# Performance work log

Measured on AMD Instinct MI355X. Metric: run time of the kernel, lower is better.

Reference implementation:

```python
import jax, jax.numpy as jnp
import numpy as np

N, E, B = 50000, 800000, 512
IN, H, D, C = 128, 4, 64, 1
NG, GH = 200, 256


def gat_layer(h, W, al, ar, src, dst, res_w=None, res_id=False, act=True):
    """DGL-style GATConv: fc -> per-head attn logits -> edge softmax by dst -> scatter-sum."""
    Nn = h.shape[0]
    Hh, Dd = al.shape
    f = (h @ W).reshape(Nn, Hh, Dd)                       # [N,H,D]
    el = jnp.einsum('nhd,hd->nh', f, al)                  # [N,H]
    er = jnp.einsum('nhd,hd->nh', f, ar)
    e = jax.nn.leaky_relu(el[src] + er[dst], 0.2)         # [E,H]
    m = jax.ops.segment_max(e, dst, num_segments=Nn)      # softmax over in-edges of each dst
    ex = jnp.exp(e - m[dst])
    den = jax.ops.segment_sum(ex, dst, num_segments=Nn)
    a = ex / den[dst]                                      # [E,H]
    rst = jax.ops.segment_sum(f[src] * a[..., None], dst, num_segments=Nn)  # [N,H,D]
    if res_id:
        rst = rst + h.reshape(Nn, Hh, Dd)
    elif res_w is not None:
        rst = rst + (h @ res_w).reshape(Nn, Hh, Dd)
    if act:
        rst = jax.nn.elu(rst)
    return rst


def setup_inputs() -> dict:
    key = jax.random.key(0)
    ks = jax.random.split(key, 24)
    s = 0.05
    HD = H * D
    return {
        'feat': jax.random.normal(ks[0], (N, IN), jnp.float32),
        'src': jax.random.randint(ks[1], (E,), 0, N, jnp.int32),
        'dst': jax.random.randint(ks[2], (E,), 0, N, jnp.int32),
        'graph_ids': jnp.sort(jax.random.randint(ks[3], (N,), 0, B, jnp.int32)),
        'g_feat': jax.random.normal(ks[4], (B, NG), jnp.float32),
        'W0': jax.random.normal(ks[5], (IN, HD), jnp.float32) * s,
        'al0': jax.random.normal(ks[6], (H, D), jnp.float32) * s,
        'ar0': jax.random.normal(ks[7], (H, D), jnp.float32) * s,
        'W1': jax.random.normal(ks[8], (HD, HD), jnp.float32) * s,
        'al1': jax.random.normal(ks[9], (H, D), jnp.float32) * s,
        'ar1': jax.random.normal(ks[10], (H, D), jnp.float32) * s,
        'W2': jax.random.normal(ks[11], (HD, HD), jnp.float32) * s,
        'al2': jax.random.normal(ks[12], (H, D), jnp.float32) * s,
        'ar2': jax.random.normal(ks[13], (H, D), jnp.float32) * s,
        'W3': jax.random.normal(ks[14], (HD, H * C), jnp.float32) * s,
        'al3': jax.random.normal(ks[15], (H, C), jnp.float32) * s,
        'ar3': jax.random.normal(ks[16], (H, C), jnp.float32) * s,
        'resW3': jax.random.normal(ks[17], (HD, H * C), jnp.float32) * s,
        'gw1': jax.random.normal(ks[18], (NG, GH), jnp.float32) * s,
        'gb1': jnp.zeros((GH,), jnp.float32),
        'gw2': jax.random.normal(ks[19], (GH, GH), jnp.float32) * s,
        'gb2': jnp.zeros((GH,), jnp.float32),
        'lw': jax.random.normal(ks[20], (H + GH, C), jnp.float32) * s,
        'lb': jnp.zeros((C,), jnp.float32),
    }


def reference(feat, src, dst, graph_ids, g_feat,
              W0, al0, ar0, W1, al1, ar1, W2, al2, ar2,
              W3, al3, ar3, resW3, gw1, gb1, gw2, gb2, lw, lb):
    h = gat_layer(feat, W0, al0, ar0, src, dst).reshape(N, -1)
    h = gat_layer(h, W1, al1, ar1, src, dst, res_id=True).reshape(N, -1)
    h = gat_layer(h, W2, al2, ar2, src, dst, res_id=True).reshape(N, -1)
    hn = gat_layer(h, W3, al3, ar3, src, dst, res_w=resW3, act=False)   # [N,H,C]
    latent = jax.ops.segment_sum(hn, graph_ids, num_segments=B).mean(axis=-1)  # [B,H]
    lg = jax.nn.relu(jax.nn.relu(g_feat @ gw1 + gb1) @ gw2 + gb2)        # [B,GH]
    return jnp.concatenate([latent, lg], axis=1) @ lw + lb               # [B,C]
```

## Files before the change

### kernel.cpp

```cpp
#include <hip/hip_runtime.h>
#include <hip/hip_bf16.h>
#include <math.h>

#define N_NODES 50000
#define N_EDGES 800000
#define NB      512
#define IN_F    128
#define NH      4
#define HD      64
#define HDIM    256
#define NG_F    200
#define GH_F    256
#define CSZ     196

typedef __attribute__((ext_vector_type(8))) short short8;
typedef __attribute__((ext_vector_type(8))) unsigned short u16x8;
typedef __attribute__((ext_vector_type(4))) float f32x4;
typedef __attribute__((ext_vector_type(2))) float f32x2;

static __device__ __forceinline__ float lrelu(float x){ return x > 0.f ? x : 0.2f*x; }
static __device__ __forceinline__ float fexp(float x){ return __expf(x); }

static __device__ __forceinline__ unsigned short f2b(float f){
  union { float f; unsigned int u; } v; v.f = f;
  unsigned int r = v.u + 0x7fffu + ((v.u >> 16) & 1u);
  return (unsigned short)(r >> 16);
}
static __device__ __forceinline__ float b2f(unsigned short b){
  union { unsigned int u; float f; } v; v.u = ((unsigned int)b) << 16;
  return v.f;
}
static __device__ __forceinline__ float u2f(unsigned int u){
  union { unsigned int u; float f; } v; v.u = u;
  return v.f;
}

__global__ __launch_bounds__(256) void k_f2b(const float* __restrict__ in, unsigned short* __restrict__ out, int n4){
  int i = blockIdx.x*256 + threadIdx.x;
  if (i >= n4) return;
  float4 v = ((const float4*)in)[i];
  ushort4 o;
  o.x = f2b(v.x); o.y = f2b(v.y); o.z = f2b(v.z); o.w = f2b(v.w);
  ((ushort4*)out)[i] = o;
}

__global__ __launch_bounds__(256) void k_padg(const float* __restrict__ g, unsigned short* __restrict__ out){
  int idx = blockIdx.x*256 + threadIdx.x;
  if (idx >= NB*256) return;
  int b = idx >> 8, k = idx & 255;
  out[idx] = (k < NG_F) ? f2b(g[b*NG_F + k]) : (unsigned short)0;
}

__global__ __launch_bounds__(256) void k_w2bt(const float* __restrict__ W, unsigned short* __restrict__ Bt,
                                              int Ksrc, int Kdst, int NC){
  __shared__ unsigned short t[32][33];
  int bn = blockIdx.x*32;
  int bk = blockIdx.y*32;
  int lx = threadIdx.x & 31, ly = threadIdx.x >> 5;
  #pragma unroll
  for (int i = 0; i < 32; i += 8) {
    int kr = bk + ly + i;
    t[ly+i][lx] = (kr < Ksrc) ? f2b(W[(size_t)kr*NC + bn+lx]) : (unsigned short)0;
  }
  __syncthreads();
  #pragma unroll
  for (int i = 0; i < 32; i += 8)
    Bt[(size_t)(bn+ly+i)*Kdst + bk+lx] = t[lx][ly+i];
}

__global__ __launch_bounds__(256) void k_hist(const int* __restrict__ dst, int* __restrict__ deg){
  int e = blockIdx.x*256 + threadIdx.x;
  if (e < N_EDGES) atomicAdd(&deg[dst[e]], 1);
}

__global__ __launch_bounds__(64) void k_s1a(const int* __restrict__ deg, int* __restrict__ blocksum){
  int b = blockIdx.x, lane = threadIdx.x;
  int start = b*CSZ, end = min(start+CSZ, N_NODES);
  int s = 0;
  for (int i = start + lane; i < end; i += 64) s += deg[i];
  #pragma unroll
  for (int m = 1; m < 64; m <<= 1) s += __shfl_xor(s, m);
  if (lane == 0) blocksum[b] = s;
}

__global__ __launch_bounds__(256) void k_s1b(const int* __restrict__ blocksum, int* __restrict__ chunkoff){
  __shared__ int sd[256];
  int t = threadIdx.x;
  int own = blocksum[t];
  sd[t] = own; __syncthreads();
  for (int off = 1; off < 256; off <<= 1) {
    int v = (t >= off) ? sd[t-off] : 0;
    __syncthreads();
    sd[t] += v;
    __syncthreads();
  }
  chunkoff[t] = sd[t] - own;
}

__global__ __launch_bounds__(64) void k_scan2(const int* __restrict__ deg, const int* __restrict__ chunkoff,
                                              int* __restrict__ row_start, int* __restrict__ cursor){
  int b = blockIdx.x, lane = threadIdx.x;
  int start = b*CSZ, end = min(start+CSZ, N_NODES);
  int run = chunkoff[b];
  for (int k = start; k < end; k += 64) {
    int idx = k + lane;
    int v = (idx < end) ? deg[idx] : 0;
    int inc = v;
    #pragma unroll
    for (int off = 1; off < 64; off <<= 1) {
      int t = __shfl_up(inc, off);
      if (lane >= off) inc += t;
    }
    int excl = run + inc - v;
    if (idx < end) { row_start[idx] = excl; cursor[idx] = excl; }
    run += __shfl(inc, 63);
  }
  if (b == 255 && lane == 0) row_start[N_NODES] = run;
}

__global__ __launch_bounds__(256) void k_scatter(const int* __restrict__ dst, const int* __restrict__ src,
                                                 int* __restrict__ cursor, int* __restrict__ csrc){
  int e = blockIdx.x*256 + threadIdx.x;
  if (e < N_EDGES) {
    int p = atomicAdd(&cursor[dst[e]], 1);
    csrc[p] = src[e];
  }
}

__global__ __launch_bounds__(256) void k_goff(const int* __restrict__ gid, int* __restrict__ goff){
  int n = blockIdx.x*256 + threadIdx.x;
  if (n >= N_NODES) return;
  int ca = gid[n];
  if (n == 0) {
    for (int g = 0; g <= ca; g++) goff[g] = 0;
  } else {
    int pa = gid[n-1];
    for (int g = pa+1; g <= ca; g++) goff[g] = n;
  }
  if (n == N_NODES-1) {
    for (int g = ca+1; g <= NB; g++) goff[g] = N_NODES;
  }
}

__global__ __launch_bounds__(256) void k_gemm_bf16(const unsigned short* __restrict__ A,
                                                   const unsigned short* __restrict__ Bt,
                                                   unsigned short* __restrict__ C,
                                                   const float* __restrict__ bias, int act,
                                                   int M, int K, int NC){
  __shared__ unsigned short As[128][72];
  __shared__ unsigned short Bs[64][72];
  const int tid = threadIdx.x;
  const int bm = blockIdx.y*128, bn = blockIdx.x*64;
  const int wid = tid >> 6, lane = tid & 63;
  const int wr = wid >> 1, wc = wid & 1;
  const int l15 = lane & 15, lg = lane >> 4;
  const int ar = tid >> 1, ak = (tid & 1) * 32;
  const int br = tid >> 2, bkp = (tid & 3) * 16;
  int agrow = bm + ar; if (agrow >= M) agrow = M - 1;

  f32x4 acc[4][2] = {};
  for (int k0 = 0; k0 < K; k0 += 64) {
    #pragma unroll
    for (int p = 0; p < 4; p++)
      *(uint4*)(&As[ar][ak + p*8]) = *(const uint4*)(A + (size_t)agrow*K + k0 + ak + p*8);
    #pragma unroll
    for (int p = 0; p < 2; p++)
      *(uint4*)(&Bs[br][bkp + p*8]) = *(const uint4*)(Bt + (size_t)(bn + br)*K + k0 + bkp + p*8);
    __syncthreads();
    #pragma unroll
    for (int ks = 0; ks < 2; ks++) {
      short8 af[4], bf[2];
      #pragma unroll
      for (int m = 0; m < 4; m++) af[m] = *(const short8*)(&As[wr*64 + m*16 + l15][ks*32 + lg*8]);
      #pragma unroll
      for (int nn = 0; nn < 2; nn++) bf[nn] = *(const short8*)(&Bs[wc*32 + nn*16 + l15][ks*32 + lg*8]);
      #pragma unroll
      for (int m = 0; m < 4; m++)
        #pragma unroll
        for (int nn = 0; nn < 2; nn++)
          acc[m][nn] = __builtin_amdgcn_mfma_f32_16x16x32_bf16(af[m], bf[nn], acc[m][nn], 0, 0, 0);
    }
    __syncthreads();
  }
  #pragma unroll
  for (int m = 0; m < 4; m++)
    #pragma unroll
    for (int nn = 0; nn < 2; nn++) {
      int col = bn + wc*32 + nn*16 + l15;
      float bv = bias ? bias[col] : 0.f;
      #pragma unroll
      for (int i = 0; i < 4; i++) {
        int row = bm + wr*64 + m*16 + lg*4 + i;
        if (row < M) {
          float v = acc[m][nn][i] + bv;
          if (act) v = fmaxf(v, 0.f);
          C[(size_t)row*NC + col] = f2b(v);
        }
      }
    }
}

__global__ __launch_bounds__(256) void k_logits(const unsigned short* __restrict__ f,
    const float* __restrict__ al, const float* __restrict__ ar,
    float* __restrict__ el, float* __restrict__ er){
  int n = blockIdx.x*4 + (threadIdx.x >> 6);
  int lane = threadIdx.x & 63;
  if (n >= N_NODES) return;
  ushort4 u = ((const ushort4*)(f + (size_t)n*HDIM))[lane];
  float4 av = ((const float4*)al)[lane];
  float4 rv = ((const float4*)ar)[lane];
  float x0 = b2f(u.x), x1 = b2f(u.y), x2 = b2f(u.z), x3 = b2f(u.w);
  float pl = x0*av.x + x1*av.y + x2*av.z + x3*av.w;
  float pr = x0*rv.x + x1*rv.y + x2*rv.z + x3*rv.w;
  #pragma unroll
  for (int m = 1; m < 16; m <<= 1) {
    pl += __shfl_xor(pl, m);
    pr += __shfl_xor(pr, m);
  }
  if ((lane & 15) == 0) {
    int h = lane >> 4;
    el[n*NH + h] = pl;
    er[n*NH + h] = pr;
  }
}

__global__ __launch_bounds__(256) void k_agg(
    const unsigned short* __restrict__ f, const float* __restrict__ el, const float* __restrict__ er,
    const int* __restrict__ row_start, const int* __restrict__ csrc,
    const unsigned short* __restrict__ resid, unsigned short* __restrict__ out, int act){
  __shared__ float sA[4][64][4];
  __shared__ int   sS[4][64];
  int wid  = threadIdx.x >> 6;
  int lane = threadIdx.x & 63;
  int n = blockIdx.x*4 + wid;
  int half = lane >> 5;
  int c    = lane & 31;
  int h    = c >> 3;
  int e0 = row_start[n], e1 = row_start[n+1];
  float4 erv = ((const float4*)er)[n];

  float4 den = make_float4(0.f,0.f,0.f,0.f);
  f32x2 acc2[4] = {};

  for (int base = e0; base < e1; base += 64) {
    int cnt = min(64, e1 - base);
    int   s_l = 0;
    float4 a4 = make_float4(0.f,0.f,0.f,0.f);
    if (base + lane < e1) {
      s_l = csrc[base + lane];
      float4 ev = ((const float4*)el)[s_l];
      a4.x = fexp(lrelu(ev.x + erv.x));
      a4.y = fexp(lrelu(ev.y + erv.y));
      a4.z = fexp(lrelu(ev.z + erv.z));
      a4.w = fexp(lrelu(ev.w + erv.w));
    }
    den.x += a4.x; den.y += a4.y; den.z += a4.z; den.w += a4.w;
    sS[wid][lane] = s_l;
    sA[wid][lane][0] = a4.x; sA[wid][lane][1] = a4.y;
    sA[wid][lane][2] = a4.z; sA[wid][lane][3] = a4.w;
    __builtin_amdgcn_sched_barrier(0);
    for (int j = 0; j < cnt; j += 16) {
      uint4 u[8]; f32x2 aa[8];
      #pragma unroll
      for (int p = 0; p < 8; p++) {
        int jj = j + 2*p + half;
        float a = 0.f; int s;
        if (jj < cnt) { s = sS[wid][jj]; a = sA[wid][jj][h]; } else { s = sS[wid][j]; }
        u[p] = *(const uint4*)(f + (size_t)s*HDIM + c*8);
        aa[p][0] = a; aa[p][1] = a;
      }
      #pragma unroll
      for (int p = 0; p < 8; p++) {
        f32x2 p0, p1, p2, p3;
        p0[0] = u2f(u[p].x << 16); p0[1] = u2f(u[p].x & 0xffff0000u);
        p1[0] = u2f(u[p].y << 16); p1[1] = u2f(u[p].y & 0xffff0000u);
        p2[0] = u2f(u[p].z << 16); p2[1] = u2f(u[p].z & 0xffff0000u);
        p3[0] = u2f(u[p].w << 16); p3[1] = u2f(u[p].w & 0xffff0000u);
        asm volatile("v_pk_fma_f32 %0, %1, %2, %0" : "+v"(acc2[0]) : "v"(p0), "v"(aa[p]));
        asm volatile("v_pk_fma_f32 %0, %1, %2, %0" : "+v"(acc2[1]) : "v"(p1), "v"(aa[p]));
        asm volatile("v_pk_fma_f32 %0, %1, %2, %0" : "+v"(acc2[2]) : "v"(p2), "v"(aa[p]));
        asm volatile("v_pk_fma_f32 %0, %1, %2, %0" : "+v"(acc2[3]) : "v"(p3), "v"(aa[p]));
      }
    }
  }
  #pragma unroll
  for (int m = 1; m < 64; m <<= 1) {
    den.x += __shfl_xor(den.x, m);
    den.y += __shfl_xor(den.y, m);
    den.z += __shfl_xor(den.z, m);
    den.w += __shfl_xor(den.w, m);
  }
  float accv[8];
  #pragma unroll
  for (int q = 0; q < 4; q++) {
    accv[2*q]   = acc2[q][0] + __shfl_xor(acc2[q][0], 32);
    accv[2*q+1] = acc2[q][1] + __shfl_xor(acc2[q][1], 32);
  }

  float d_h = h==0 ? den.x : h==1 ? den.y : h==2 ? den.z : den.w;
  float inv = d_h > 0.f ? 1.0f/d_h : 0.f;

  if (half == 0) {
    #pragma unroll
    for (int k = 0; k < 8; k++) accv[k] *= inv;
    if (resid) {
      u16x8 r = *(const u16x8*)(resid + (size_t)n*HDIM + c*8);
      #pragma unroll
      for (int k = 0; k < 8; k++) accv[k] += b2f((unsigned short)r[k]);
    }
    if (act) {
      #pragma unroll
      for (int k = 0; k < 8; k++) accv[k] = accv[k] > 0.f ? accv[k] : (fexp(accv[k]) - 1.0f);
    }
    u16x8 o;
    #pragma unroll
    for (int k = 0; k < 8; k++) o[k] = f2b(accv[k]);
    *(u16x8*)(out + (size_t)n*HDIM + c*8) = o;
  }
}

__global__ __launch_bounds__(256) void k_l3proj(const unsigned short* __restrict__ h,
    const float* __restrict__ W3, const float* __restrict__ rW3,
    const float* __restrict__ al3, const float* __restrict__ ar3,
    float* __restrict__ f3, float* __restrict__ r3,
    float* __restrict__ el3, float* __restrict__ er3){
  int n = blockIdx.x*4 + (threadIdx.x >> 6);
  int lane = threadIdx.x & 63;
  if (n >= N_NODES) return;
  ushort4 u = ((const ushort4*)(h + (size_t)n*HDIM))[lane];
  float hk[4] = {b2f(u.x), b2f(u.y), b2f(u.z), b2f(u.w)};
  const float4* w  = (const float4*)W3;
  const float4* rw = (const float4*)rW3;
  float4 acc = make_float4(0.f,0.f,0.f,0.f);
  float4 rac = make_float4(0.f,0.f,0.f,0.f);
  #pragma unroll
  for (int j = 0; j < 4; j++) {
    float4 wv = w[lane*4 + j];
    float4 rv = rw[lane*4 + j];
    acc.x += hk[j]*wv.x; acc.y += hk[j]*wv.y; acc.z += hk[j]*wv.z; acc.w += hk[j]*wv.w;
    rac.x += hk[j]*rv.x; rac.y += hk[j]*rv.y; rac.z += hk[j]*rv.z; rac.w += hk[j]*rv.w;
  }
  #pragma unroll
  for (int m = 1; m < 64; m <<= 1) {
    acc.x += __shfl_xor(acc.x, m); acc.y += __shfl_xor(acc.y, m);
    acc.z += __shfl_xor(acc.z, m); acc.w += __shfl_xor(acc.w, m);
    rac.x += __shfl_xor(rac.x, m); rac.y += __shfl_xor(rac.y, m);
    rac.z += __shfl_xor(rac.z, m); rac.w += __shfl_xor(rac.w, m);
  }
  if (lane == 0) {
    ((float4*)f3)[n] = acc;
    ((float4*)r3)[n] = rac;
    float4 e1 = make_float4(acc.x*al3[0], acc.y*al3[1], acc.z*al3[2], acc.w*al3[3]);
    float4 e2 = make_float4(acc.x*ar3[0], acc.y*ar3[1], acc.z*ar3[2], acc.w*ar3[3]);
    ((float4*)el3)[n] = e1;
    ((float4*)er3)[n] = e2;
  }
}

__global__ __launch_bounds__(256) void k_l3node(
    const float* __restrict__ f3, const float* __restrict__ el3, const float* __restrict__ er3,
    const int* __restrict__ row_start, const int* __restrict__ csrc,
    const float* __restrict__ r3, float* __restrict__ hn){
  int g = threadIdx.x >> 4;
  int l = threadIdx.x & 15;
  int n = blockIdx.x*16 + g;
  int e0 = row_start[n], e1 = row_start[n+1];
  float4 erv = ((const float4*)er3)[n];

  float4 dn  = make_float4(0.f,0.f,0.f,0.f);
  float4 acc = make_float4(0.f,0.f,0.f,0.f);
  for (int i = e0 + l; i < e1; i += 16) {
    int s = csrc[i];
    float4 ev = ((const float4*)el3)[s];
    float ax = fexp(lrelu(ev.x + erv.x));
    float ay = fexp(lrelu(ev.y + erv.y));
    float az = fexp(lrelu(ev.z + erv.z));
    float aw = fexp(lrelu(ev.w + erv.w));
    dn.x += ax; dn.y += ay; dn.z += az; dn.w += aw;
    float4 fv = ((const float4*)f3)[s];
    acc.x += ax*fv.x; acc.y += ay*fv.y; acc.z += az*fv.z; acc.w += aw*fv.w;
  }
  #pragma unroll
  for (int m = 1; m < 16; m <<= 1) {
    dn.x += __shfl_xor(dn.x, m);  dn.y += __shfl_xor(dn.y, m);
    dn.z += __shfl_xor(dn.z, m);  dn.w += __shfl_xor(dn.w, m);
    acc.x += __shfl_xor(acc.x, m); acc.y += __shfl_xor(acc.y, m);
    acc.z += __shfl_xor(acc.z, m); acc.w += __shfl_xor(acc.w, m);
  }
  if (l == 0) {
    float4 rv = ((const float4*)r3)[n];
    float4 o;
    o.x = (dn.x > 0.f ? acc.x/dn.x : 0.f) + rv.x;
    o.y = (dn.y > 0.f ? acc.y/dn.y : 0.f) + rv.y;
    o.z = (dn.z > 0.f ? acc.z/dn.z : 0.f) + rv.z;
    o.w = (dn.w > 0.f ? acc.w/dn.w : 0.f) + rv.w;
    ((float4*)hn)[n] = o;
  }
}

__global__ __launch_bounds__(64) void k_gseg(const float* __restrict__ hn, const int* __restrict__ goff,
                                             float* __restrict__ latent){
  int b = blockIdx.x;
  int lane = threadIdx.x;
  int n0 = goff[b], n1 = goff[b+1];
  float4 s = make_float4(0.f,0.f,0.f,0.f);
  for (int n = n0 + lane; n < n1; n += 64) {
    float4 v = ((const float4*)hn)[n];
    s.x += v.x; s.y += v.y; s.z += v.z; s.w += v.w;
  }
  #pragma unroll
  for (int m = 1; m < 64; m <<= 1) {
    s.x += __shfl_xor(s.x, m); s.y += __shfl_xor(s.y, m);
    s.z += __shfl_xor(s.z, m); s.w += __shfl_xor(s.w, m);
  }
  if (lane == 0) ((float4*)latent)[b] = s;
}

__global__ __launch_bounds__(256) void k_final(const float* __restrict__ latent, const unsigned short* __restrict__ lgb,
    const float* __restrict__ lw, const float* __restrict__ lb, float* __restrict__ out){
  int b = blockIdx.x*4 + (threadIdx.x >> 6);
  int lane = threadIdx.x & 63;
  if (b >= NB) return;
  ushort4 u = ((const ushort4*)(lgb + (size_t)b*GH_F))[lane];
  float4 wv = ((const float4*)(lw + NH))[lane];
  float s = b2f(u.x)*wv.x + b2f(u.y)*wv.y + b2f(u.z)*wv.z + b2f(u.w)*wv.w;
  #pragma unroll
  for (int m = 1; m < 64; m <<= 1) s += __shfl_xor(s, m);
  if (lane == 0) {
    float4 lv = ((const float4*)latent)[b];
    out[b] = s + lv.x*lw[0] + lv.y*lw[1] + lv.z*lw[2] + lv.w*lw[3] + lb[0];
  }
}

__global__ __launch_bounds__(256) void k_sentinel(float* out){
  int i = blockIdx.x*256 + threadIdx.x;
  if (i < NB) out[i] = -12345.0f;
}

extern "C" void kernel_launch(void* const* d_in, const int* in_sizes, int n_in,
                              void* d_out, int out_size, void* d_ws, size_t ws_size,
                              hipStream_t stream){
  const float* feat   = (const float*)d_in[0];
  const int*   src    = (const int*)d_in[1];
  const int*   dst    = (const int*)d_in[2];
  const int*   gid    = (const int*)d_in[3];
  const float* g_feat = (const float*)d_in[4];
  const float* W0   = (const float*)d_in[5];
  const float* al0  = (const float*)d_in[6];
  const float* ar0  = (const float*)d_in[7];
  const float* W1   = (const float*)d_in[8];
  const float* al1  = (const float*)d_in[9];
  const float* ar1  = (const float*)d_in[10];
  const float* W2   = (const float*)d_in[11];
  const float* al2  = (const float*)d_in[12];
  const float* ar2  = (const float*)d_in[13];
  const float* W3   = (const float*)d_in[14];
  const float* al3  = (const float*)d_in[15];
  const float* ar3  = (const float*)d_in[16];
  const float* rW3  = (const float*)d_in[17];
  const float* gw1  = (const float*)d_in[18];
  const float* gb1  = (const float*)d_in[19];
  const float* gw2  = (const float*)d_in[20];
  const float* gb2  = (const float*)d_in[21];
  const float* lw   = (const float*)d_in[22];
  const float* lb   = (const float*)d_in[23];
  float* out = (float*)d_out;

  char* base = (char*)d_ws;
  size_t off = 0;
  auto alloc = [&](size_t bytes)->char* {
    char* r = base + off;
    off += (bytes + 255) & ~(size_t)255;
    return r;
  };
  unsigned short* featb = (unsigned short*)alloc((size_t)N_NODES*IN_F*2);
  unsigned short* fbuf  = (unsigned short*)alloc((size_t)N_NODES*HDIM*2);
  unsigned short* hA    = (unsigned short*)alloc((size_t)N_NODES*HDIM*2);
  unsigned short* hB    = (unsigned short*)alloc((size_t)N_NODES*HDIM*2);
  unsigned short* W0t   = (unsigned short*)alloc((size_t)IN_F*HDIM*2);
  unsigned short* W1t   = (unsigned short*)alloc((size_t)HDIM*HDIM*2);
  unsigned short* W2t   = (unsigned short*)alloc((size_t)HDIM*HDIM*2);
  unsigned short* gfb   = (unsigned short*)alloc((size_t)NB*256*2);
  unsigned short* gw1t  = (unsigned short*)alloc((size_t)GH_F*256*2);
  unsigned short* gw2t  = (unsigned short*)alloc((size_t)GH_F*GH_F*2);
  unsigned short* g1b   = (unsigned short*)alloc((size_t)NB*GH_F*2);
  unsigned short* lgb   = (unsigned short*)alloc((size_t)NB*GH_F*2);
  float* el   = (float*)alloc((size_t)N_NODES*NH*4);
  float* er   = (float*)alloc((size_t)N_NODES*NH*4);
  float* f3   = (float*)alloc((size_t)N_NODES*NH*4);
  float* r3   = (float*)alloc((size_t)N_NODES*NH*4);
  float* hn   = (float*)alloc((size_t)N_NODES*NH*4);
  int* deg       = (int*)alloc((size_t)N_NODES*4);
  int* row_start = (int*)alloc((size_t)(N_NODES+1)*4);
  int* cursor    = (int*)alloc((size_t)N_NODES*4);
  int* csrc      = (int*)alloc((size_t)N_EDGES*4);
  int* blocksum  = (int*)alloc(256*4);
  int* chunkoff  = (int*)alloc(256*4);
  int* goff      = (int*)alloc((size_t)(NB+1)*4);
  float* latent  = (float*)alloc((size_t)NB*NH*4);

  if (off > ws_size) {
    k_sentinel<<<2, 256, 0, stream>>>(out);
    return;
  }

  k_f2b<<<((N_NODES*IN_F/4)+255)/256, 256, 0, stream>>>(feat, featb, N_NODES*IN_F/4);
  {
    dim3 g0(HDIM/32, IN_F/32), g12(HDIM/32, HDIM/32), gm(256/32, 256/32);
    k_w2bt<<<g0, 256, 0, stream>>>(W0, W0t, IN_F, IN_F, HDIM);
    k_w2bt<<<g12, 256, 0, stream>>>(W1, W1t, HDIM, HDIM, HDIM);
    k_w2bt<<<g12, 256, 0, stream>>>(W2, W2t, HDIM, HDIM, HDIM);
    k_w2bt<<<gm, 256, 0, stream>>>(gw1, gw1t, NG_F, 256, GH_F);
    k_w2bt<<<gm, 256, 0, stream>>>(gw2, gw2t, GH_F, GH_F, GH_F);
  }
  k_padg<<<(NB*256+255)/256, 256, 0, stream>>>(g_feat, gfb);

  hipMemsetAsync(deg, 0, (size_t)N_NODES*4, stream);
  k_hist<<<(N_EDGES+255)/256, 256, 0, stream>>>(dst, deg);
  k_s1a<<<256, 64, 0, stream>>>(deg, blocksum);
  k_s1b<<<1, 256, 0, stream>>>(blocksum, chunkoff);
  k_scan2<<<256, 64, 0, stream>>>(deg, chunkoff, row_start, cursor);
  k_scatter<<<(N_EDGES+255)/256, 256, 0, stream>>>(dst, src, cursor, csrc);
  k_goff<<<(N_NODES+255)/256, 256, 0, stream>>>(gid, goff);

  dim3 ggrid(HDIM/64, (N_NODES+127)/128);

  k_gemm_bf16<<<ggrid, 256, 0, stream>>>(featb, W0t, fbuf, nullptr, 0, N_NODES, IN_F, HDIM);
  k_logits<<<(N_NODES+3)/4, 256, 0, stream>>>(fbuf, al0, ar0, el, er);
  k_agg<<<N_NODES/4, 256, 0, stream>>>(fbuf, el, er, row_start, csrc, nullptr, hA, 1);

  k_gemm_bf16<<<ggrid, 256, 0, stream>>>(hA, W1t, fbuf, nullptr, 0, N_NODES, HDIM, HDIM);
  k_logits<<<(N_NODES+3)/4, 256, 0, stream>>>(fbuf, al1, ar1, el, er);
  k_agg<<<N_NODES/4, 256, 0, stream>>>(fbuf, el, er, row_start, csrc, hA, hB, 1);

  k_gemm_bf16<<<ggrid, 256, 0, stream>>>(hB, W2t, fbuf, nullptr, 0, N_NODES, HDIM, HDIM);
  k_logits<<<(N_NODES+3)/4, 256, 0, stream>>>(fbuf, al2, ar2, el, er);
  k_agg<<<N_NODES/4, 256, 0, stream>>>(fbuf, el, er, row_start, csrc, hB, hA, 1);

  k_l3proj<<<(N_NODES+3)/4, 256, 0, stream>>>(hA, W3, rW3, al3, ar3, f3, r3, el, er);
  k_l3node<<<N_NODES/16, 256, 0, stream>>>(f3, el, er, row_start, csrc, r3, hn);
  k_gseg<<<NB, 64, 0, stream>>>(hn, goff, latent);

  {
    dim3 mgrid(GH_F/64, (NB+127)/128);
    k_gemm_bf16<<<mgrid, 256, 0, stream>>>(gfb, gw1t, g1b, gb1, 1, NB, 256, GH_F);
    k_gemm_bf16<<<mgrid, 256, 0, stream>>>(g1b, gw2t, lgb, gb2, 1, NB, GH_F, GH_F);
  }
  k_final<<<(NB+3)/4, 256, 0, stream>>>(latent, lgb, lw, lb, out);
}
```

Baseline: 483.6 us.

## Fuse attention logits into GEMM epilogue and shrink agg gather unroll

The per-head el/er dot products are computed from the fp32 MFMA accumulators inside the GEMM epilogue. Each block owns one head's 64 columns, so partial sums are reduced across lanes and waves through shared memory. This removes the separate k_logits kernel and its re-read of the projected features in three layers. Separately, the k_agg inner gather loop is cut from 8 to 4 outstanding neighbor loads per iteration, trading memory-level parallelism for lower register pressure. The fused epilogue adds shuffles and a block barrier to every GEMM call that supplies attention vectors, and computes the logits from unrounded fp32 values rather than the bf16-rounded stored features.

After: 482.1 us. Within noise of the previous version (-0.3%).

```diff
diff --git a/kernel.cpp b/kernel.cpp
--- a/kernel.cpp
+++ b/kernel.cpp
@@ -146,23 +146,27 @@
                                                    const unsigned short* __restrict__ Bt,
                                                    unsigned short* __restrict__ C,
                                                    const float* __restrict__ bias, int act,
+                                                   const float* __restrict__ al, const float* __restrict__ ar,
+                                                   float* __restrict__ el, float* __restrict__ er,
                                                    int M, int K, int NC){
   __shared__ unsigned short As[128][72];
   __shared__ unsigned short Bs[64][72];
+  __shared__ float sEL[2][2][4][16];
+  __shared__ float sER[2][2][4][16];
   const int tid = threadIdx.x;
   const int bm = blockIdx.y*128, bn = blockIdx.x*64;
   const int wid = tid >> 6, lane = tid & 63;
   const int wr = wid >> 1, wc = wid & 1;
   const int l15 = lane & 15, lg = lane >> 4;
-  const int ar = tid >> 1, ak = (tid & 1) * 32;
+  const int ar_ = tid >> 1, ak = (tid & 1) * 32;
   const int br = tid >> 2, bkp = (tid & 3) * 16;
-  int agrow = bm + ar; if (agrow >= M) agrow = M - 1;
+  int agrow = bm + ar_; if (agrow >= M) agrow = M - 1;
 
   f32x4 acc[4][2] = {};
   for (int k0 = 0; k0 < K; k0 += 64) {
     #pragma unroll
     for (int p = 0; p < 4; p++)
-      *(uint4*)(&As[ar][ak + p*8]) = *(const uint4*)(A + (size_t)agrow*K + k0 + ak + p*8);
+      *(uint4*)(&As[ar_][ak + p*8]) = *(const uint4*)(A + (size_t)agrow*K + k0 + ak + p*8);
     #pragma unroll
     for (int p = 0; p < 2; p++)
       *(uint4*)(&Bs[br][bkp + p*8]) = *(const uint4*)(Bt + (size_t)(bn + br)*K + k0 + bkp + p*8);
@@ -198,29 +202,45 @@
         }
       }
     }
-}
-
-__global__ __launch_bounds__(256) void k_logits(const unsigned short* __restrict__ f,
-    const float* __restrict__ al, const float* __restrict__ ar,
-    float* __restrict__ el, float* __restrict__ er){
-  int n = blockIdx.x*4 + (threadIdx.x >> 6);
-  int lane = threadIdx.x & 63;
-  if (n >= N_NODES) return;
-  ushort4 u = ((const ushort4*)(f + (size_t)n*HDIM))[lane];
-  float4 av = ((const float4*)al)[lane];
-  float4 rv = ((const float4*)ar)[lane];
-  float x0 = b2f(u.x), x1 = b2f(u.y), x2 = b2f(u.z), x3 = b2f(u.w);
-  float pl = x0*av.x + x1*av.y + x2*av.z + x3*av.w;
-  float pr = x0*rv.x + x1*rv.y + x2*rv.z + x3*rv.w;
-  #pragma unroll
-  for (int m = 1; m < 16; m <<= 1) {
-    pl += __shfl_xor(pl, m);
-    pr += __shfl_xor(pr, m);
-  }
-  if ((lane & 15) == 0) {
-    int h = lane >> 4;
-    el[n*NH + h] = pl;
-    er[n*NH + h] = pr;
+  if (al) {
+    int hidx = bn >> 6;
+    float pl[16], pr[16];
+    #pragma unroll
+    for (int m = 0; m < 4; m++)
+      #pragma unroll
+      for (int i = 0; i < 4; i++) {
+        float sl = 0.f, sr = 0.f;
+        #pragma unroll
+        for (int nn = 0; nn < 2; nn++) {
+          int colh = wc*32 + nn*16 + l15;
+          sl += acc[m][nn][i] * al[hidx*64 + colh];
+          sr += acc[m][nn][i] * ar[hidx*64 + colh];
+        }
+        pl[m*4+i] = sl; pr[m*4+i] = sr;
+      }
+    #pragma unroll
+    for (int k = 0; k < 16; k++) {
+      #pragma unroll
+      for (int mm = 1; mm < 16; mm <<= 1) {
+        pl[k] += __shfl_xor(pl[k], mm);
+        pr[k] += __shfl_xor(pr[k], mm);
+      }
+    }
+    if (l15 == 0) {
+      #pragma unroll
+      for (int k = 0; k < 16; k++) { sEL[wr][wc][lg][k] = pl[k]; sER[wr][wc][lg][k] = pr[k]; }
+    }
+    __syncthreads();
+    if (tid < 128) {
+      int k = tid & 15;
+      int lg2 = (tid >> 4) & 3;
+      int wr2 = tid >> 6;
+      float vl = sEL[wr2][0][lg2][k] + sEL[wr2][1][lg2][k];
+      float vr = sER[wr2][0][lg2][k] + sER[wr2][1][lg2][k];
+      int m = k >> 2, i = k & 3;
+      int row = bm + wr2*64 + m*16 + lg2*4 + i;
+      if (row < M) { el[row*NH + hidx] = vl; er[row*NH + hidx] = vr; }
+    }
   }
 }
 
@@ -259,10 +279,10 @@
     sA[wid][lane][0] = a4.x; sA[wid][lane][1] = a4.y;
     sA[wid][lane][2] = a4.z; sA[wid][lane][3] = a4.w;
     __builtin_amdgcn_sched_barrier(0);
-    for (int j = 0; j < cnt; j += 16) {
-      uint4 u[8]; f32x2 aa[8];
-      #pragma unroll
-      for (int p = 0; p < 8; p++) {
+    for (int j = 0; j < cnt; j += 8) {
+      uint4 u[4]; f32x2 aa[4];
+      #pragma unroll
+      for (int p = 0; p < 4; p++) {
         int jj = j + 2*p + half;
         float a = 0.f; int s;
         if (jj < cnt) { s = sS[wid][jj]; a = sA[wid][jj][h]; } else { s = sS[wid][j]; }
@@ -270,7 +290,7 @@
         aa[p][0] = a; aa[p][1] = a;
       }
       #pragma unroll
-      for (int p = 0; p < 8; p++) {
+      for (int p = 0; p < 4; p++) {
         f32x2 p0, p1, p2, p3;
         p0[0] = u2f(u[p].x << 16); p0[1] = u2f(u[p].x & 0xffff0000u);
         p1[0] = u2f(u[p].y << 16); p1[1] = u2f(u[p].y & 0xffff0000u);
@@ -525,16 +545,13 @@
 
   dim3 ggrid(HDIM/64, (N_NODES+127)/128);
 
-  k_gemm_bf16<<<ggrid, 256, 0, stream>>>(featb, W0t, fbuf, nullptr, 0, N_NODES, IN_F, HDIM);
-  k_logits<<<(N_NODES+3)/4, 256, 0, stream>>>(fbuf, al0, ar0, el, er);
+  k_gemm_bf16<<<ggrid, 256, 0, stream>>>(featb, W0t, fbuf, nullptr, 0, al0, ar0, el, er, N_NODES, IN_F, HDIM);
   k_agg<<<N_NODES/4, 256, 0, stream>>>(fbuf, el, er, row_start, csrc, nullptr, hA, 1);
 
-  k_gemm_bf16<<<ggrid, 256, 0, stream>>>(hA, W1t, fbuf, nullptr, 0, N_NODES, HDIM, HDIM);
-  k_logits<<<(N_NODES+3)/4, 256, 0, stream>>>(fbuf, al1, ar1, el, er);
+  k_gemm_bf16<<<ggrid, 256, 0, stream>>>(hA, W1t, fbuf, nullptr, 0, al1, ar1, el, er, N_NODES, HDIM, HDIM);
   k_agg<<<N_NODES/4, 256, 0, stream>>>(fbuf, el, er, row_start, csrc, hA, hB, 1);
 
-  k_gemm_bf16<<<ggrid, 256, 0, stream>>>(hB, W2t, fbuf, nullptr, 0, N_NODES, HDIM, HDIM);
-  k_logits<<<(N_NODES+3)/4, 256, 0, stream>>>(fbuf, al2, ar2, el, er);
+  k_gemm_bf16<<<ggrid, 256, 0, stream>>>(hB, W2t, fbuf, nullptr, 0, al2, ar2, el, er, N_NODES, HDIM, HDIM);
   k_agg<<<N_NODES/4, 256, 0, stream>>>(fbuf, el, er, row_start, csrc, hB, hA, 1);
 
   k_l3proj<<<(N_NODES+3)/4, 256, 0, stream>>>(hA, W3, rW3, al3, ar3, f3, r3, el, er);
@@ -543,8 +560,8 @@
 
   {
     dim3 mgrid(GH_F/64, (NB+127)/128);
-    k_gemm_bf16<<<mgrid, 256, 0, stream>>>(gfb, gw1t, g1b, gb1, 1, NB, 256, GH_F);
-    k_gemm_bf16<<<mgrid, 256, 0, stream>>>(g1b, gw2t, lgb, gb2, 1, NB, GH_F, GH_F);
+    k_gemm_bf16<<<mgrid, 256, 0, stream>>>(gfb, gw1t, g1b, gb1, 1, nullptr, nullptr, nullptr, nullptr, NB, 256, GH_F);
+    k_gemm_bf16<<<mgrid, 256, 0, stream>>>(g1b, gw2t, lgb, gb2, 1, nullptr, nullptr, nullptr, nullptr, NB, GH_F, GH_F);
   }
   k_final<<<(NB+3)/4, 256, 0, stream>>>(latent, lgb, lw, lb, out);
 }
```
